# Kernel optimization log

Measured on AMD Instinct MI355X. Metric: run time of the kernel, lower is better.

## Reference

```python
import jax, jax.numpy as jnp
import numpy as np
import math

N, D, H = 4096, 2048, 16
HD = D // H  # head_dim = 128


def setup_inputs() -> dict:
    key = jax.random.key(0)
    ks = jax.random.split(key, 9)
    s = 1.0 / math.sqrt(D)
    return {
        "x":  jax.random.normal(ks[0], (N, D), dtype=jnp.float32),
        "Wq": jax.random.normal(ks[1], (D, D), dtype=jnp.float32) * s,
        "bq": jax.random.normal(ks[2], (D,), dtype=jnp.float32) * s,
        "Wk": jax.random.normal(ks[3], (D, D), dtype=jnp.float32) * s,
        "bk": jax.random.normal(ks[4], (D,), dtype=jnp.float32) * s,
        "Wv": jax.random.normal(ks[5], (D, D), dtype=jnp.float32) * s,
        "bv": jax.random.normal(ks[6], (D,), dtype=jnp.float32) * s,
        "Wo": jax.random.normal(ks[7], (D, D), dtype=jnp.float32) * s,
        "bo": jax.random.normal(ks[8], (D,), dtype=jnp.float32) * s,
    }


def reference(x, Wq, bq, Wk, bk, Wv, bv, Wo, bo):
    # eqx.nn.Linear: y = W @ x + b, weight shape (out, in) -> x @ W.T + b
    q = x @ Wq.T + bq            # [N, D]
    k = x @ Wk.T + bk            # [N, D]
    v = x @ Wv.T + bv            # [N, D]
    q = q.reshape(N, H, HD).transpose(1, 0, 2)   # [H, N, hd]
    k = k.reshape(N, H, HD).transpose(1, 2, 0)   # [H, hd, N]
    v = v.reshape(N, H, HD).transpose(1, 0, 2)   # [H, N, hd]
    scale = 1.0 / math.sqrt(HD)
    scores = jnp.matmul(q * scale, k)            # [H, N, N]
    attn = jax.nn.softmax(scores, axis=-1)
    ctx = jnp.matmul(attn, v)                    # [H, N, hd]
    ctx = ctx.transpose(1, 0, 2).reshape(N, D)   # [N, D]
    return ctx @ Wo.T + bo
```

## Files before the change

### kernel.cpp

```cpp
#include <hip/hip_runtime.h>
#include <stdint.h>

#define N_TOK 4096
#define DIM   2048
#define NH    16
#define HD    128
#define NW    (DIM * DIM)

using bf16x8 = __attribute__((ext_vector_type(8))) short;
using bf16x4 = __attribute__((ext_vector_type(4))) short;
using f32x4  = __attribute__((ext_vector_type(4))) float;
using u32x2  = __attribute__((ext_vector_type(2))) unsigned int;

#if __has_builtin(__builtin_amdgcn_exp2f)
#define EXP2(x) __builtin_amdgcn_exp2f(x)
#else
#define EXP2(x) exp2f(x)
#endif

__device__ inline unsigned short f2bf(float f) {
  union { float f; unsigned u; } v; v.f = f;
  unsigned r = v.u + 0x7FFFu + ((v.u >> 16) & 1u);
  return (unsigned short)(r >> 16);
}
__device__ inline float bf2f(unsigned short u) {
  union { unsigned u; float f; } v; v.u = ((unsigned)u) << 16; return v.f;
}
__device__ inline f32x4 mfma16(bf16x8 a, bf16x8 b, f32x4 c) {
  return __builtin_amdgcn_mfma_f32_16x16x32_bf16(a, b, c, 0, 0, 0);
}
__device__ inline void gll16(const unsigned short* g, unsigned short* l) {
  __builtin_amdgcn_global_load_lds(
      (const __attribute__((address_space(1))) void*)g,
      (__attribute__((address_space(3))) void*)l, 16, 0, 0);
}

__device__ inline unsigned cvtpk_bf16(float lo, float hi) {
  unsigned r;
  asm("v_cvt_pk_bf16_f32 %0, %1, %2" : "=v"(r) : "v"(lo), "v"(hi));
  return r;
}

__device__ inline u32x2 pl32swap(unsigned a, unsigned b) {
#if __has_builtin(__builtin_amdgcn_permlane32_swap)
  return __builtin_amdgcn_permlane32_swap(a, b, false, false);
#else
  int lane = threadIdx.x & 63;
  unsigned as = (unsigned)__shfl_xor((int)a, 32);
  unsigned bs = (unsigned)__shfl_xor((int)b, 32);
  u32x2 r;
  r.x = (lane & 32) ? bs : a;
  r.y = (lane & 32) ? b : as;
  return r;
#endif
}
__device__ inline u32x2 pl16swap(unsigned a, unsigned b) {
#if __has_builtin(__builtin_amdgcn_permlane16_swap)
  return __builtin_amdgcn_permlane16_swap(a, b, false, false);
#else
  int lane = threadIdx.x & 63;
  unsigned as = (unsigned)__shfl_xor((int)a, 16);
  unsigned bs = (unsigned)__shfl_xor((int)b, 16);
  u32x2 r;
  r.x = (lane & 16) ? bs : a;
  r.y = (lane & 16) ? b : as;
  return r;
#endif
}

__global__ __launch_bounds__(256)
void cvt_bf16(const float* __restrict__ src, unsigned short* __restrict__ dst, int n) {
  int i = blockIdx.x * 256 + threadIdx.x;
  if (i * 8 >= n) return;
  const float4* s = (const float4*)src + (size_t)i * 2;
  float4 a = s[0], b = s[1];
  bf16x8 o;
  o[0] = (short)f2bf(a.x); o[1] = (short)f2bf(a.y);
  o[2] = (short)f2bf(a.z); o[3] = (short)f2bf(a.w);
  o[4] = (short)f2bf(b.x); o[5] = (short)f2bf(b.y);
  o[6] = (short)f2bf(b.z); o[7] = (short)f2bf(b.w);
  *(bf16x8*)(dst + (size_t)i * 8) = o;
}

template<int OUT_MODE>
__global__ __launch_bounds__(256)
void gemm_bf16(const unsigned short* __restrict__ A, const unsigned short* __restrict__ B,
               const float* __restrict__ bias, void* __restrict__ out_, float scale) {
  __shared__ unsigned short Asl[128 * 32];
  __shared__ unsigned short Bsl[128 * 32];
  const int tid  = threadIdx.x;
  const int lane = tid & 63, w = tid >> 6;
  const int wy = w >> 1, wx = w & 1;
  const int lr = lane & 15, quad = lane >> 4;
  const int m0 = blockIdx.y * 128, n0 = blockIdx.x * 128;

  const f32x4 vzero = {0.f, 0.f, 0.f, 0.f};
  f32x4 acc[4][4];
#pragma unroll
  for (int i = 0; i < 4; ++i)
#pragma unroll
    for (int j = 0; j < 4; ++j) acc[i][j] = vzero;

  for (int k0 = 0; k0 < DIM; k0 += 32) {
    __syncthreads();
#pragma unroll
    for (int i = 0; i < 2; ++i) {
      int ch = tid + i * 256;
      int r = ch >> 2, cc = ch & 3;
      gll16(&A[(size_t)(m0 + r) * DIM + k0 + cc * 8], &Asl[ch * 8]);
      gll16(&B[(size_t)(n0 + r) * DIM + k0 + cc * 8], &Bsl[ch * 8]);
    }
    __syncthreads();

    bf16x8 af[4], bfv[4];
#pragma unroll
    for (int mb = 0; mb < 4; ++mb)
      af[mb] = *(const bf16x8*)&Asl[(wy * 64 + mb * 16 + lr) * 32 + quad * 8];
#pragma unroll
    for (int nb = 0; nb < 4; ++nb)
      bfv[nb] = *(const bf16x8*)&Bsl[(wx * 64 + nb * 16 + lr) * 32 + quad * 8];
#pragma unroll
    for (int mb = 0; mb < 4; ++mb)
#pragma unroll
      for (int nb = 0; nb < 4; ++nb)
        acc[mb][nb] = mfma16(af[mb], bfv[nb], acc[mb][nb]);
  }

#pragma unroll
  for (int mb = 0; mb < 4; ++mb)
#pragma unroll
    for (int nb = 0; nb < 4; ++nb) {
      int gn = n0 + wx * 64 + nb * 16 + lr;
      int gm_base = m0 + wy * 64 + mb * 16 + quad * 4;
      float bs = bias[gn];
      if constexpr (OUT_MODE == 2) {
        bf16x4 pk;
#pragma unroll
        for (int r = 0; r < 4; ++r) pk[r] = (short)f2bf((acc[mb][nb][r] + bs) * scale);
        *(bf16x4*)&((unsigned short*)out_)[(size_t)gn * N_TOK + gm_base] = pk;
      } else {
#pragma unroll
        for (int r = 0; r < 4; ++r) {
          float v = (acc[mb][nb][r] + bs) * scale;
          if constexpr (OUT_MODE == 1)
            ((float*)out_)[(size_t)(gm_base + r) * DIM + gn] = v;
          else
            ((unsigned short*)out_)[(size_t)(gm_base + r) * DIM + gn] = f2bf(v);
        }
      }
    }
}

__global__ __launch_bounds__(256, 1)
void flash_attn(const unsigned short* __restrict__ Q,
                const unsigned short* __restrict__ K,
                const unsigned short* __restrict__ Vt,
                unsigned short* __restrict__ ctx) {
  constexpr int LDK = 136;
  constexpr int LDV = 72;
  constexpr int NT  = N_TOK / 64;
  __shared__ unsigned short Ksl[64 * LDK];
  __shared__ unsigned short VTsl[128 * LDV];

  const int tid  = threadIdx.x;
  const int lane = tid & 63, w = tid >> 6;
  const int lr = lane & 15, quad = lane >> 4;
  const int hoff = blockIdx.y * HD;
  const int q0   = blockIdx.x * 256;
  const int qw   = q0 + w * 64;

  bf16x8 qf[4][4];
#pragma unroll
  for (int mb = 0; mb < 4; ++mb)
#pragma unroll
    for (int c = 0; c < 4; ++c)
      qf[mb][c] = *(const bf16x8*)&Q[(size_t)(qw + mb * 16 + lr) * DIM + hoff + c * 32 + quad * 8];

  const f32x4 vzero = {0.f, 0.f, 0.f, 0.f};
  f32x4 o[4][8];
  float l_acc[4] = {0.f, 0.f, 0.f, 0.f};
#pragma unroll
  for (int mb = 0; mb < 4; ++mb)
#pragma unroll
    for (int nb = 0; nb < 8; ++nb) o[mb][nb] = vzero;

  bf16x8 kreg[4], vreg[4];
  auto load_tile = [&](int kt) {
    int kbase = kt * 64;
#pragma unroll
    for (int i = 0; i < 4; ++i) {
      int ch = tid + i * 256;
      kreg[i] = *(const bf16x8*)&K[(size_t)(kbase + (ch >> 4)) * DIM + hoff + (ch & 15) * 8];
      vreg[i] = *(const bf16x8*)&Vt[(size_t)(hoff + (ch >> 3)) * N_TOK + kbase + (ch & 7) * 8];
    }
  };
  load_tile(0);

  for (int kt = 0; kt < NT; ++kt) {
    __syncthreads();
#pragma unroll
    for (int i = 0; i < 4; ++i) {
      int ch = tid + i * 256;
      *(bf16x8*)&Ksl[(ch >> 4) * LDK + (ch & 15) * 8] = kreg[i];
      *(bf16x8*)&VTsl[(ch >> 3) * LDV + (ch & 7) * 8] = vreg[i];
    }
    __syncthreads();
    if (kt + 1 < NT) load_tile(kt + 1);

    f32x4 s[4][4];
#pragma unroll
    for (int mb = 0; mb < 4; ++mb)
#pragma unroll
      for (int nf = 0; nf < 4; ++nf) s[mb][nf] = vzero;
#pragma unroll
    for (int nf = 0; nf < 4; ++nf)
#pragma unroll
      for (int c = 0; c < 4; ++c) {
        bf16x8 kf = *(const bf16x8*)&Ksl[(nf * 16 + lr) * LDK + c * 32 + quad * 8];
#pragma unroll
        for (int mb = 0; mb < 4; ++mb) s[mb][nf] = mfma16(kf, qf[mb][c], s[mb][nf]);
      }

    bf16x8 pf[4][2];
#pragma unroll
    for (int mb = 0; mb < 4; ++mb) {
      unsigned W[4][2];
      float lp = 0.f;
#pragma unroll
      for (int nf = 0; nf < 4; ++nf) {
        float e0 = EXP2(s[mb][nf][0]);
        float e1 = EXP2(s[mb][nf][1]);
        float e2 = EXP2(s[mb][nf][2]);
        float e3 = EXP2(s[mb][nf][3]);
        lp += (e0 + e1) + (e2 + e3);
        W[nf][0] = cvtpk_bf16(e0, e1);
        W[nf][1] = cvtpk_bf16(e2, e3);
      }
      l_acc[mb] += lp;
#pragma unroll
      for (int ki = 0; ki < 2; ++ki) {
        u32x2 a0  = pl32swap(W[2 * ki][0], W[2 * ki + 1][0]);
        u32x2 t02 = pl16swap(a0.x, a0.y);
        u32x2 a1  = pl32swap(W[2 * ki][1], W[2 * ki + 1][1]);
        u32x2 t13 = pl16swap(a1.x, a1.y);
        union { unsigned u[4]; bf16x8 v; } pu;
        pu.u[0] = t02.x; pu.u[1] = t13.x; pu.u[2] = t02.y; pu.u[3] = t13.y;
        pf[mb][ki] = pu.v;
      }
    }

#pragma unroll
    for (int nb = 0; nb < 8; ++nb)
#pragma unroll
      for (int ki = 0; ki < 2; ++ki) {
        bf16x8 vf = *(const bf16x8*)&VTsl[(nb * 16 + lr) * LDV + ki * 32 + quad * 8];
#pragma unroll
        for (int mb = 0; mb < 4; ++mb) o[mb][nb] = mfma16(pf[mb][ki], vf, o[mb][nb]);
      }
  }

#pragma unroll
  for (int mb = 0; mb < 4; ++mb) {
    float t = l_acc[mb];
    t += __shfl_xor(t, 16);
    t += __shfl_xor(t, 32);
    l_acc[mb] = t;
  }
#pragma unroll
  for (int mb = 0; mb < 4; ++mb)
#pragma unroll
    for (int r = 0; r < 4; ++r) {
      float Lr = __shfl(l_acc[mb], quad * 4 + r);
      float inv = 1.0f / Lr;
      int gq = qw + mb * 16 + quad * 4 + r;
#pragma unroll
      for (int nb = 0; nb < 8; ++nb)
        ctx[(size_t)gq * DIM + hoff + nb * 16 + lr] = f2bf(o[mb][nb][r] * inv);
    }
}

extern "C" void kernel_launch(void* const* d_in, const int* in_sizes, int n_in,
                              void* d_out, int out_size, void* d_ws, size_t ws_size,
                              hipStream_t stream) {
  (void)in_sizes; (void)n_in; (void)out_size; (void)ws_size;
  const float* x  = (const float*)d_in[0];
  const float* Wq = (const float*)d_in[1];
  const float* bq = (const float*)d_in[2];
  const float* Wk = (const float*)d_in[3];
  const float* bk = (const float*)d_in[4];
  const float* Wv = (const float*)d_in[5];
  const float* bv = (const float*)d_in[6];
  const float* Wo = (const float*)d_in[7];
  const float* bo = (const float*)d_in[8];

  const size_t NE = (size_t)N_TOK * DIM;
  unsigned short* xb  = (unsigned short*)d_ws;
  unsigned short* Wqb = xb + NE;
  unsigned short* Wkb = Wqb + NW;
  unsigned short* Wvb = Wkb + NW;
  unsigned short* Wob = Wvb + NW;
  unsigned short* Qb  = Wob + NW;
  unsigned short* Kb  = Qb + NE;
  unsigned short* Vtb = Kb + NE;

  cvt_bf16<<<4096, 256, 0, stream>>>(x,  xb,  (int)NE);
  cvt_bf16<<<2048, 256, 0, stream>>>(Wq, Wqb, NW);
  cvt_bf16<<<2048, 256, 0, stream>>>(Wk, Wkb, NW);
  cvt_bf16<<<2048, 256, 0, stream>>>(Wv, Wvb, NW);
  cvt_bf16<<<2048, 256, 0, stream>>>(Wo, Wob, NW);

  dim3 gemm_grid(DIM / 128, N_TOK / 128);
  const float qscale = 1.4426950408889634f * 0.08838834764831845f;

  gemm_bf16<0><<<gemm_grid, 256, 0, stream>>>(xb, Wqb, bq, Qb, qscale);
  gemm_bf16<0><<<gemm_grid, 256, 0, stream>>>(xb, Wkb, bk, Kb, 1.0f);
  gemm_bf16<2><<<gemm_grid, 256, 0, stream>>>(xb, Wvb, bv, Vtb, 1.0f);

  unsigned short* ctxb = xb;
  flash_attn<<<dim3(N_TOK / 256, NH), 256, 0, stream>>>(Qb, Kb, Vtb, ctxb);

  gemm_bf16<1><<<gemm_grid, 256, 0, stream>>>(ctxb, Wob, bo, (float*)d_out, 1.0f);
}
```

Baseline: 491.1 us.

## Software-pipeline attention loop so softmax overlaps next tile's QK and PV MFMAs

Restructures the flash attention inner loop so the QK^T MFMAs for tile kt and the PV MFMAs for tile kt-1 are issued together, with the softmax (exp2 and bf16 packing) for tile kt done afterwards. K is double-buffered and V^T triple-buffered in LDS, which lets each iteration drop to a single __syncthreads. s_setprio is raised around the MFMA block so waves with matrix work get scheduling priority while other waves run exp. This is meant to overlap the VALU softmax with the matrix cores. The cost is more LDS and more live registers for s and pf carried across iterations.

```diff
diff --git a/kernel.cpp b/kernel.cpp
--- a/kernel.cpp
+++ b/kernel.cpp
@@ -159,8 +159,8 @@
   constexpr int LDK = 136;
   constexpr int LDV = 72;
   constexpr int NT  = N_TOK / 64;
-  __shared__ unsigned short Ksl[64 * LDK];
-  __shared__ unsigned short VTsl[128 * LDV];
+  __shared__ unsigned short Ksl[2][64 * LDK];
+  __shared__ unsigned short VTsl[3][128 * LDV];
 
   const int tid  = threadIdx.x;
   const int lane = tid & 63, w = tid >> 6;
@@ -194,20 +194,19 @@
       vreg[i] = *(const bf16x8*)&Vt[(size_t)(hoff + (ch >> 3)) * N_TOK + kbase + (ch & 7) * 8];
     }
   };
-  load_tile(0);
-
-  for (int kt = 0; kt < NT; ++kt) {
-    __syncthreads();
+  auto stage = [&](int kb, int vb) {
 #pragma unroll
     for (int i = 0; i < 4; ++i) {
       int ch = tid + i * 256;
-      *(bf16x8*)&Ksl[(ch >> 4) * LDK + (ch & 15) * 8] = kreg[i];
-      *(bf16x8*)&VTsl[(ch >> 3) * LDV + (ch & 7) * 8] = vreg[i];
-    }
-    __syncthreads();
-    if (kt + 1 < NT) load_tile(kt + 1);
-
-    f32x4 s[4][4];
+      *(bf16x8*)&Ksl[kb][(ch >> 4) * LDK + (ch & 15) * 8] = kreg[i];
+      *(bf16x8*)&VTsl[vb][(ch >> 3) * LDV + (ch & 7) * 8] = vreg[i];
+    }
+  };
+
+  f32x4 s[4][4];
+  bf16x8 pf[4][2];
+
+  auto qk = [&](int kb) {
 #pragma unroll
     for (int mb = 0; mb < 4; ++mb)
 #pragma unroll
@@ -216,12 +215,24 @@
     for (int nf = 0; nf < 4; ++nf)
 #pragma unroll
       for (int c = 0; c < 4; ++c) {
-        bf16x8 kf = *(const bf16x8*)&Ksl[(nf * 16 + lr) * LDK + c * 32 + quad * 8];
+        bf16x8 kf = *(const bf16x8*)&Ksl[kb][(nf * 16 + lr) * LDK + c * 32 + quad * 8];
 #pragma unroll
         for (int mb = 0; mb < 4; ++mb) s[mb][nf] = mfma16(kf, qf[mb][c], s[mb][nf]);
       }
-
-    bf16x8 pf[4][2];
+  };
+
+  auto pv = [&](int vb) {
+#pragma unroll
+    for (int nb = 0; nb < 8; ++nb)
+#pragma unroll
+      for (int ki = 0; ki < 2; ++ki) {
+        bf16x8 vf = *(const bf16x8*)&VTsl[vb][(nb * 16 + lr) * LDV + ki * 32 + quad * 8];
+#pragma unroll
+        for (int mb = 0; mb < 4; ++mb) o[mb][nb] = mfma16(pf[mb][ki], vf, o[mb][nb]);
+      }
+  };
+
+  auto softmax = [&]() {
 #pragma unroll
     for (int mb = 0; mb < 4; ++mb) {
       unsigned W[4][2];
@@ -248,16 +259,26 @@
         pf[mb][ki] = pu.v;
       }
     }
-
-#pragma unroll
-    for (int nb = 0; nb < 8; ++nb)
-#pragma unroll
-      for (int ki = 0; ki < 2; ++ki) {
-        bf16x8 vf = *(const bf16x8*)&VTsl[(nb * 16 + lr) * LDV + ki * 32 + quad * 8];
-#pragma unroll
-        for (int mb = 0; mb < 4; ++mb) o[mb][nb] = mfma16(pf[mb][ki], vf, o[mb][nb]);
-      }
+  };
+
+  load_tile(0);
+  stage(0, 0);
+  __syncthreads();
+  load_tile(1);
+  qk(0);
+  softmax();
+
+  for (int kt = 1; kt < NT; ++kt) {
+    stage(kt & 1, kt % 3);
+    __syncthreads();
+    if (kt + 1 < NT) load_tile(kt + 1);
+    __builtin_amdgcn_s_setprio(1);
+    qk(kt & 1);
+    pv((kt - 1) % 3);
+    __builtin_amdgcn_s_setprio(0);
+    softmax();
   }
+  pv((NT - 1) % 3);
 
 #pragma unroll
   for (int mb = 0; mb < 4; ++mb) {
```

New measurement: 507.3 us. +3.3%, slower.

## Rewrite GEMM with 256x128x64 tiles, triple-buffered LDS pipeline and XOR swizzle

Applied to the files above, without the earlier changes.

The projection GEMM moves to 512-thread blocks computing 256x128 tiles with BK=64. Global-to-LDS loads go into a three-stage buffer and are issued two tiles ahead, split into halves interleaved with MFMA work, using raw barriers and explicit vmcnt waits. LDS rows use an XOR swizzle to avoid bank conflicts, and the MFMA sections run at raised wave priority. The aim is to hide global load latency and cut the sync-bound stalls of the old single-buffer loop, at the cost of 144KB of LDS, which allows only one block per CU, and more delicate wait-count logic.

```diff
diff --git a/kernel.cpp b/kernel.cpp
--- a/kernel.cpp
+++ b/kernel.cpp
@@ -33,6 +33,11 @@
   __builtin_amdgcn_global_load_lds(
       (const __attribute__((address_space(1))) void*)g,
       (__attribute__((address_space(3))) void*)l, 16, 0, 0);
+}
+__device__ inline void wgbar() {
+  asm volatile("" ::: "memory");
+  __builtin_amdgcn_s_barrier();
+  asm volatile("" ::: "memory");
 }
 
 __device__ inline unsigned cvtpk_bf16(float lo, float hi) {
@@ -83,16 +88,20 @@
 }
 
 template<int OUT_MODE>
-__global__ __launch_bounds__(256)
+__global__ __launch_bounds__(512, 2)
 void gemm_bf16(const unsigned short* __restrict__ A, const unsigned short* __restrict__ B,
                const float* __restrict__ bias, void* __restrict__ out_, float scale) {
-  __shared__ unsigned short Asl[128 * 32];
-  __shared__ unsigned short Bsl[128 * 32];
+  constexpr int BM = 256, BN = 128, BK = 64;
+  constexpr int NKT = DIM / BK;
+  __shared__ unsigned short Asl[3][BM * BK];
+  __shared__ unsigned short Bsl[3][BN * BK];
+
   const int tid  = threadIdx.x;
-  const int lane = tid & 63, w = tid >> 6;
-  const int wy = w >> 1, wx = w & 1;
+  const int lane = tid & 63;
+  const int w    = tid >> 6;
+  const int wm = w >> 1, wn = w & 1;
   const int lr = lane & 15, quad = lane >> 4;
-  const int m0 = blockIdx.y * 128, n0 = blockIdx.x * 128;
+  const int m0 = blockIdx.y * BM, n0 = blockIdx.x * BN;
 
   const f32x4 vzero = {0.f, 0.f, 0.f, 0.f};
   f32x4 acc[4][4];
@@ -101,37 +110,101 @@
 #pragma unroll
     for (int j = 0; j < 4; ++j) acc[i][j] = vzero;
 
-  for (int k0 = 0; k0 < DIM; k0 += 32) {
-    __syncthreads();
-#pragma unroll
-    for (int i = 0; i < 2; ++i) {
-      int ch = tid + i * 256;
-      int r = ch >> 2, cc = ch & 3;
-      gll16(&A[(size_t)(m0 + r) * DIM + k0 + cc * 8], &Asl[ch * 8]);
-      gll16(&B[(size_t)(n0 + r) * DIM + k0 + cc * 8], &Bsl[ch * 8]);
-    }
-    __syncthreads();
-
-    bf16x8 af[4], bfv[4];
-#pragma unroll
-    for (int mb = 0; mb < 4; ++mb)
-      af[mb] = *(const bf16x8*)&Asl[(wy * 64 + mb * 16 + lr) * 32 + quad * 8];
-#pragma unroll
-    for (int nb = 0; nb < 4; ++nb)
-      bfv[nb] = *(const bf16x8*)&Bsl[(wx * 64 + nb * 16 + lr) * 32 + quad * 8];
+  size_t asrc[4]; int aldst[4];
+  size_t bsrc[2]; int bldst[2];
+#pragma unroll
+  for (int i = 0; i < 4; ++i) {
+    int ch = tid + i * 512;
+    int row = ch >> 3, cc = ch & 7;
+    int gcc = cc ^ (row & 7);
+    asrc[i]  = (size_t)(m0 + row) * DIM + gcc * 8;
+    aldst[i] = ch * 8;
+  }
+#pragma unroll
+  for (int i = 0; i < 2; ++i) {
+    int ch = tid + i * 512;
+    int row = ch >> 3, cc = ch & 7;
+    int gcc = cc ^ (row & 7);
+    bsrc[i]  = (size_t)(n0 + row) * DIM + gcc * 8;
+    bldst[i] = ch * 8;
+  }
+  auto stage_half = [&](int buf, int k0, int half) {
+    int a0 = half * 2;
+    gll16(&A[asrc[a0] + k0],     &Asl[buf][aldst[a0]]);
+    gll16(&A[asrc[a0 + 1] + k0], &Asl[buf][aldst[a0 + 1]]);
+    gll16(&B[bsrc[half] + k0],   &Bsl[buf][bldst[half]]);
+  };
+
+  auto lda = [&](int buf, int ks, bf16x8* af) {
+#pragma unroll
+    for (int mb = 0; mb < 4; ++mb) {
+      int row  = wm * 64 + mb * 16 + lr;
+      int slot = (ks * 4 + quad) ^ (row & 7);
+      af[mb] = *(const bf16x8*)&Asl[buf][row * 64 + slot * 8];
+    }
+  };
+  auto ldb = [&](int buf, int ks, bf16x8* bfv) {
+#pragma unroll
+    for (int nb = 0; nb < 4; ++nb) {
+      int row  = wn * 64 + nb * 16 + lr;
+      int slot = (ks * 4 + quad) ^ (row & 7);
+      bfv[nb] = *(const bf16x8*)&Bsl[buf][row * 64 + slot * 8];
+    }
+  };
+  auto mm = [&](bf16x8* af, bf16x8* bfv) {
+    __builtin_amdgcn_s_setprio(1);
 #pragma unroll
     for (int mb = 0; mb < 4; ++mb)
 #pragma unroll
       for (int nb = 0; nb < 4; ++nb)
         acc[mb][nb] = mfma16(af[mb], bfv[nb], acc[mb][nb]);
+    __builtin_amdgcn_s_setprio(0);
+  };
+
+  stage_half(0, 0, 0);  stage_half(0, 0, 1);
+  stage_half(1, BK, 0); stage_half(1, BK, 1);
+  asm volatile("s_waitcnt vmcnt(6)" ::: "memory");
+  wgbar();
+
+  for (int t = 0; t < NKT - 2; ++t) {
+    const int buf = t % 3, sb = (t + 2) % 3, sk = (t + 2) * BK;
+    bf16x8 af[4], bfv[4];
+    lda(buf, 0, af); ldb(buf, 0, bfv);
+    stage_half(sb, sk, 0);
+    wgbar();
+    mm(af, bfv);
+    wgbar();
+    lda(buf, 1, af); ldb(buf, 1, bfv);
+    stage_half(sb, sk, 1);
+    asm volatile("s_waitcnt vmcnt(6)" ::: "memory");
+    wgbar();
+    mm(af, bfv);
+    wgbar();
+  }
+  {
+    const int buf = (NKT - 2) % 3;
+    bf16x8 af[4], bfv[4];
+    lda(buf, 0, af); ldb(buf, 0, bfv);
+    wgbar(); mm(af, bfv); wgbar();
+    lda(buf, 1, af); ldb(buf, 1, bfv);
+    asm volatile("s_waitcnt vmcnt(0)" ::: "memory");
+    wgbar(); mm(af, bfv); wgbar();
+  }
+  {
+    const int buf = (NKT - 1) % 3;
+    bf16x8 af[4], bfv[4];
+    lda(buf, 0, af); ldb(buf, 0, bfv);
+    mm(af, bfv);
+    lda(buf, 1, af); ldb(buf, 1, bfv);
+    mm(af, bfv);
   }
 
 #pragma unroll
   for (int mb = 0; mb < 4; ++mb)
 #pragma unroll
     for (int nb = 0; nb < 4; ++nb) {
-      int gn = n0 + wx * 64 + nb * 16 + lr;
-      int gm_base = m0 + wy * 64 + mb * 16 + quad * 4;
+      int gn = n0 + wn * 64 + nb * 16 + lr;
+      int gm_base = m0 + wm * 64 + mb * 16 + quad * 4;
       float bs = bias[gn];
       if constexpr (OUT_MODE == 2) {
         bf16x4 pk;
@@ -309,15 +382,15 @@
   cvt_bf16<<<2048, 256, 0, stream>>>(Wv, Wvb, NW);
   cvt_bf16<<<2048, 256, 0, stream>>>(Wo, Wob, NW);
 
-  dim3 gemm_grid(DIM / 128, N_TOK / 128);
+  dim3 gemm_grid(DIM / 128, N_TOK / 256);
   const float qscale = 1.4426950408889634f * 0.08838834764831845f;
 
-  gemm_bf16<0><<<gemm_grid, 256, 0, stream>>>(xb, Wqb, bq, Qb, qscale);
-  gemm_bf16<0><<<gemm_grid, 256, 0, stream>>>(xb, Wkb, bk, Kb, 1.0f);
-  gemm_bf16<2><<<gemm_grid, 256, 0, stream>>>(xb, Wvb, bv, Vtb, 1.0f);
+  gemm_bf16<0><<<gemm_grid, 512, 0, stream>>>(xb, Wqb, bq, Qb, qscale);
+  gemm_bf16<0><<<gemm_grid, 512, 0, stream>>>(xb, Wkb, bk, Kb, 1.0f);
+  gemm_bf16<2><<<gemm_grid, 512, 0, stream>>>(xb, Wvb, bv, Vtb, 1.0f);
 
   unsigned short* ctxb = xb;
   flash_attn<<<dim3(N_TOK / 256, NH), 256, 0, stream>>>(Qb, Kb, Vtb, ctxb);
 
-  gemm_bf16<1><<<gemm_grid, 256, 0, stream>>>(ctxb, Wob, bo, (float*)d_out, 1.0f);
-}
+  gemm_bf16<1><<<gemm_grid, 512, 0, stream>>>(ctxb, Wob, bo, (float*)d_out, 1.0f);
+}
```

Result: faster. 445.5 us (-9.3%).
